# Performance work log

Measured on AMD Instinct MI355X. Metric: run time of the kernel, lower is better.

## Reference

```python
import jax, jax.numpy as jnp
import numpy as np

NINP = 850
NHID = 850
T = 128
B = 256
INITRANGE = 0.04
# DARTS published recurrent cell genotype
GENO_RECURRENT = [("sigmoid", 0), ("relu", 1), ("relu", 1), ("identity", 1),
                  ("tanh", 2), ("sigmoid", 5), ("tanh", 3), ("relu", 5)]
GENO_CONCAT = [1, 2, 3, 4, 5, 6, 7, 8]

ACT = {
    "tanh": jnp.tanh,
    "relu": jax.nn.relu,
    "sigmoid": jax.nn.sigmoid,
    "identity": lambda x: x,
}


def setup_inputs() -> dict:
    key = jax.random.key(0)
    ks = jax.random.split(key, 8)
    u = lambda k, s: jax.random.uniform(k, s, jnp.float32, -INITRANGE, INITRANGE)
    return {
        "inputs": jax.random.normal(ks[0], (T, B, NINP), jnp.float32),
        "hidden": jnp.zeros((1, B, NHID), jnp.float32),
        "W0_U": u(ks[1], (2 * NHID, 2 * NHID)),
        "W0_sigma": u(ks[2], (2 * NHID,)),
        "W0_V": u(ks[3], (2 * NHID, 2 * NHID)),
        "Ws_U": u(ks[4], (8, NHID, NHID)),
        "Ws_sigma": u(ks[5], (8, NHID)),
        "Ws_V": u(ks[6], (8, 2 * NHID, 2 * NHID)),
    }


def _lowrank_square(x, U, sig, V):
    # row == col: W = U @ diag(sig) @ V
    return ((x @ U) * sig) @ V


def _lowrank_wide(x, U, sig, V):
    # row < col (row=NHID, col=2*NHID): rectangular diag embeds rank=row into col dims
    t = (x @ U) * sig                               # [B, NHID]
    t = jnp.pad(t, ((0, 0), (0, V.shape[0] - t.shape[-1])))  # [B, 2*NHID]
    return t @ V                                    # [B, 2*NHID]


def _cell(x, h_prev, W0_U, W0_sigma, W0_V, Ws_U, Ws_sigma, Ws_V):
    xh = jnp.concatenate([x, h_prev], axis=-1)      # [B, 2*NHID]
    ch0 = _lowrank_square(xh, W0_U, W0_sigma, W0_V)  # [B, 2*NHID]
    c0 = jax.nn.sigmoid(ch0[:, :NHID])
    h0 = jnp.tanh(ch0[:, NHID:])
    s0 = h_prev + c0 * (h0 - h_prev)
    states = [s0]
    for i, (name, pred) in enumerate(GENO_RECURRENT):
        sp = states[pred]
        ch = _lowrank_wide(sp, Ws_U[i], Ws_sigma[i], Ws_V[i])
        c = jax.nn.sigmoid(ch[:, :NHID])
        hh = ACT[name](ch[:, NHID:])
        states.append(sp + c * (hh - sp))
    return jnp.mean(jnp.stack([states[i] for i in GENO_CONCAT], axis=-1), axis=-1)


def reference(inputs, hidden, W0_U, W0_sigma, W0_V, Ws_U, Ws_sigma, Ws_V):
    def step(h, x):
        h_new = _cell(x, h, W0_U, W0_sigma, W0_V, Ws_U, Ws_sigma, Ws_V)
        return h_new, h_new

    _, hiddens = jax.lax.scan(step, hidden[0], inputs)   # [T, B, NHID]
    return hiddens, hiddens[-1][None]
```

## Files before the change

kernel.cpp:

```cpp
#include <hip/hip_runtime.h>

typedef unsigned short u16;
typedef unsigned int u32;
typedef __attribute__((ext_vector_type(8))) short bf16x8;
typedef __attribute__((ext_vector_type(4))) float f32x4;

#define NHID 850
#define BATCH 256
#define TSTEPS 128
#define KPAD 896
#define KPAD0 1792

#define ACT_SIG 0
#define ACT_TANH 1
#define ACT_RELU 2
#define ACT_ID 3

__device__ __forceinline__ u16 f2bf(float f) {
  u32 u = __float_as_uint(f);
  u32 r = (u + 0x7fffu + ((u >> 16) & 1u)) >> 16;
  return (u16)r;
}
__device__ __forceinline__ float sigm(float x) { return 1.f / (1.f + __expf(-x)); }
__device__ __forceinline__ float act_apply(float x, int a) {
  if (a == ACT_SIG) return sigm(x);
  if (a == ACT_TANH) return 2.f * sigm(2.f * x) - 1.f;
  if (a == ACT_RELU) return fmaxf(x, 0.f);
  return x;
}

#define GLOAD_LDS16(gsrc, ldst)                                                     \
  __builtin_amdgcn_global_load_lds((const __attribute__((address_space(1))) void*)(gsrc), \
                                   (__attribute__((address_space(3))) void*)(ldst), 16, 0, 0)

__global__ void zero_kernel(uint4* p, u32 n) {
  u32 i = blockIdx.x * blockDim.x + threadIdx.x;
  const u32 stride = gridDim.x * blockDim.x;
  const uint4 z = {0u, 0u, 0u, 0u};
  for (; i < n; i += stride) p[i] = z;
}

__global__ void convert_kernel(const float* __restrict__ x, const float* __restrict__ h0,
                               u16* __restrict__ xb, u16* __restrict__ hb) {
  const u32 NX = (u32)TSTEPS * BATCH * NHID;
  u32 i = blockIdx.x * blockDim.x + threadIdx.x;
  if (i < NX) {
    const u32 tb = i / NHID, j = i - tb * NHID;
    xb[(size_t)tb * KPAD + j] = f2bf(x[i]);
  } else if (i < NX + (u32)BATCH * NHID) {
    const u32 k = i - NX;
    const u32 b = k / NHID, j = k - b * NHID;
    hb[(size_t)b * KPAD + j] = f2bf(h0[k]);
  }
}

__global__ __launch_bounds__(256) void prew0_kernel(const float* __restrict__ U,
                                                    const float* __restrict__ sig,
                                                    const float* __restrict__ V,
                                                    u16* __restrict__ outC,
                                                    u16* __restrict__ outH) {
  const int M = 1700, N = 1700, K = 1700;
  __shared__ float sA[64][17];
  __shared__ float sB[16][65];
  const int tid = threadIdx.x;
  const int tx = tid & 15, ty = tid >> 4;
  const int m0 = blockIdx.x * 64, n0 = blockIdx.y * 64;
  float acc[4][4] = {};
  for (int kb = 0; kb < K; kb += 16) {
#pragma unroll
    for (int i = 0; i < 4; ++i) {
      const int e = tid + i * 256;
      const int r = e >> 4, c = e & 15;
      const int mm = m0 + r, kk = kb + c;
      sA[r][c] = (mm < M && kk < K) ? U[(size_t)mm * K + kk] * sig[kk] : 0.f;
    }
#pragma unroll
    for (int i = 0; i < 4; ++i) {
      const int e = tid + i * 256;
      const int r = e >> 6, c = e & 63;
      const int kk = kb + r, nn = n0 + c;
      sB[r][c] = (kk < K && nn < N) ? V[(size_t)kk * N + nn] : 0.f;
    }
    __syncthreads();
#pragma unroll
    for (int k = 0; k < 16; ++k) {
      float a[4], b[4];
#pragma unroll
      for (int i = 0; i < 4; ++i) a[i] = sA[tx * 4 + i][k];
#pragma unroll
      for (int j = 0; j < 4; ++j) b[j] = sB[k][ty * 4 + j];
#pragma unroll
      for (int i = 0; i < 4; ++i)
#pragma unroll
        for (int j = 0; j < 4; ++j) acc[i][j] += a[i] * b[j];
    }
    __syncthreads();
  }
#pragma unroll
  for (int i = 0; i < 4; ++i) {
    const int m = m0 + tx * 4 + i;
    if (m >= M) continue;
    const int rp = (m < 850) ? m : m + 46;
#pragma unroll
    for (int j = 0; j < 4; ++j) {
      const int n = n0 + ty * 4 + j;
      if (n >= N) continue;
      if (n < 850) outC[(size_t)n * KPAD0 + rp] = f2bf(acc[i][j]);
      else outH[(size_t)(n - 850) * KPAD0 + rp] = f2bf(acc[i][j]);
    }
  }
}

__global__ __launch_bounds__(256) void prewn_kernel(const float* __restrict__ Uall,
                                                    const float* __restrict__ sigall,
                                                    const float* __restrict__ Vall,
                                                    u16* __restrict__ outBase) {
  const int M = 850, N = 1700, K = 850;
  const int ndi = blockIdx.z;
  const float* U = Uall + (size_t)ndi * 850 * 850;
  const float* sig = sigall + (size_t)ndi * 850;
  const float* V = Vall + (size_t)ndi * 1700 * 1700;
  u16* outC = outBase + (size_t)ndi * 2 * KPAD * KPAD;
  u16* outH = outC + (size_t)KPAD * KPAD;
  __shared__ float sA[64][17];
  __shared__ float sB[16][65];
  const int tid = threadIdx.x;
  const int tx = tid & 15, ty = tid >> 4;
  const int m0 = blockIdx.x * 64, n0 = blockIdx.y * 64;
  float acc[4][4] = {};
  for (int kb = 0; kb < K; kb += 16) {
#pragma unroll
    for (int i = 0; i < 4; ++i) {
      const int e = tid + i * 256;
      const int r = e >> 4, c = e & 15;
      const int mm = m0 + r, kk = kb + c;
      sA[r][c] = (mm < M && kk < K) ? U[(size_t)mm * K + kk] * sig[kk] : 0.f;
    }
#pragma unroll
    for (int i = 0; i < 4; ++i) {
      const int e = tid + i * 256;
      const int r = e >> 6, c = e & 63;
      const int kk = kb + r, nn = n0 + c;
      sB[r][c] = (kk < K && nn < N) ? V[(size_t)kk * 1700 + nn] : 0.f;
    }
    __syncthreads();
#pragma unroll
    for (int k = 0; k < 16; ++k) {
      float a[4], b[4];
#pragma unroll
      for (int i = 0; i < 4; ++i) a[i] = sA[tx * 4 + i][k];
#pragma unroll
      for (int j = 0; j < 4; ++j) b[j] = sB[k][ty * 4 + j];
#pragma unroll
      for (int i = 0; i < 4; ++i)
#pragma unroll
        for (int j = 0; j < 4; ++j) acc[i][j] += a[i] * b[j];
    }
    __syncthreads();
  }
#pragma unroll
  for (int i = 0; i < 4; ++i) {
    const int m = m0 + tx * 4 + i;
    if (m >= M) continue;
#pragma unroll
    for (int j = 0; j < 4; ++j) {
      const int n = n0 + ty * 4 + j;
      if (n >= N) continue;
      if (n < 850) outC[(size_t)n * KPAD + m] = f2bf(acc[i][j]);
      else outH[(size_t)(n - 850) * KPAD + m] = f2bf(acc[i][j]);
    }
  }
}

struct NodeDesc {
  const u16* A;
  const u16* A2;
  const u16* Bc;
  const u16* Bh;
  const float* sp;
  float* outF;
  u16* outB;
  int act;
};
struct StageArgs {
  NodeDesc d[3];
  int Kt, ktA, bStride;
};

__global__ __launch_bounds__(256) void stage_kernel(StageArgs sa) {
  const NodeDesc nd = sa.d[blockIdx.z];
  __shared__ __align__(16) u16 lA[2][4096];
  __shared__ __align__(16) u16 lBc[2][4096];
  __shared__ __align__(16) u16 lBh[2][4096];
  const int tid = threadIdx.x;
  const int lane = tid & 63;
  const int w = tid >> 6;
  const int wm = (w & 1) * 32;
  const int wn = (w >> 1) * 32;
  const int m0 = blockIdx.x * 64;
  const int n0 = blockIdx.y * 64;

  f32x4 acc[2][2][2] = {};

  auto stage = [&](int buf, int kt) {
    const u16* Asrc;
    int ktl;
    if (kt < sa.ktA) { Asrc = nd.A; ktl = kt; }
    else { Asrc = nd.A2; ktl = kt - sa.ktA; }
#pragma unroll
    for (int r2 = 0; r2 < 2; ++r2) {
      const int e = tid + 256 * r2;
      const int row = e >> 3;
      const int q = (e & 7) ^ (row & 7);
      const u16* gA = Asrc + (size_t)(m0 + row) * KPAD + ktl * 64 + q * 8;
      GLOAD_LDS16(gA, &lA[buf][e * 8]);
      const u16* gBc = nd.Bc + (size_t)(n0 + row) * sa.bStride + kt * 64 + q * 8;
      GLOAD_LDS16(gBc, &lBc[buf][e * 8]);
      const u16* gBh = nd.Bh + (size_t)(n0 + row) * sa.bStride + kt * 64 + q * 8;
      GLOAD_LDS16(gBh, &lBh[buf][e * 8]);
    }
  };

  stage(0, 0);
  int cur = 0;
  for (int kt = 0; kt < sa.Kt; ++kt) {
    __syncthreads();
    if (kt + 1 < sa.Kt) stage(cur ^ 1, kt + 1);
#pragma unroll
    for (int ks = 0; ks < 2; ++ks) {
      const int kg = lane >> 4;
      bf16x8 af[2], bc[2], bh[2];
#pragma unroll
      for (int mf = 0; mf < 2; ++mf) {
        const int row = wm + mf * 16 + (lane & 15);
        const int p = (ks * 4 + kg) ^ (row & 7);
        af[mf] = *(const bf16x8*)&lA[cur][row * 64 + p * 8];
      }
#pragma unroll
      for (int nf = 0; nf < 2; ++nf) {
        const int nr = wn + nf * 16 + (lane & 15);
        const int p = (ks * 4 + kg) ^ (nr & 7);
        bc[nf] = *(const bf16x8*)&lBc[cur][nr * 64 + p * 8];
        bh[nf] = *(const bf16x8*)&lBh[cur][nr * 64 + p * 8];
      }
#pragma unroll
      for (int mf = 0; mf < 2; ++mf)
#pragma unroll
        for (int nf = 0; nf < 2; ++nf) {
          acc[0][mf][nf] = __builtin_amdgcn_mfma_f32_16x16x32_bf16(af[mf], bc[nf], acc[0][mf][nf], 0, 0, 0);
          acc[1][mf][nf] = __builtin_amdgcn_mfma_f32_16x16x32_bf16(af[mf], bh[nf], acc[1][mf][nf], 0, 0, 0);
        }
    }
    cur ^= 1;
  }

  const int colb = n0 + wn + (lane & 15);
  const int rowb = m0 + wm + ((lane >> 4) << 2);
#pragma unroll
  for (int nf = 0; nf < 2; ++nf) {
    const int j = colb + nf * 16;
    if (j >= NHID) continue;
#pragma unroll
    for (int mf = 0; mf < 2; ++mf) {
      const int mb = rowb + mf * 16;
      const f32x4 ac = acc[0][mf][nf];
      const f32x4 ah = acc[1][mf][nf];
#pragma unroll
      for (int r = 0; r < 4; ++r) {
        const int m = mb + r;
        const float c = sigm(ac[r]);
        const float hv = act_apply(ah[r], nd.act);
        const float spv = nd.sp[m * NHID + j];
        const float s = spv + c * (hv - spv);
        nd.outF[m * NHID + j] = s;
        nd.outB[(size_t)m * KPAD + j] = f2bf(s);
      }
    }
  }
}

struct FinalArgs {
  const u16* A;
  const u16* B[4];
  const float* s1; const float* s2; const float* s3;
  const float* s4; const float* s5; const float* s7;
  float* outH;
  u16* hb;
};

__global__ __launch_bounds__(256) void final_kernel(FinalArgs fa) {
  __shared__ __align__(16) u16 lA[2][4096];
  __shared__ __align__(16) u16 lB[2][4][4096];
  const int tid = threadIdx.x;
  const int lane = tid & 63;
  const int w = tid >> 6;
  const int wm = (w & 1) * 32;
  const int wn = (w >> 1) * 32;
  const int m0 = blockIdx.x * 64;
  const int n0 = blockIdx.y * 64;

  f32x4 acc[4][2][2] = {};

  auto stage = [&](int buf, int kt) {
#pragma unroll
    for (int r2 = 0; r2 < 2; ++r2) {
      const int e = tid + 256 * r2;
      const int row = e >> 3;
      const int q = (e & 7) ^ (row & 7);
      GLOAD_LDS16(fa.A + (size_t)(m0 + row) * KPAD + kt * 64 + q * 8, &lA[buf][e * 8]);
#pragma unroll
      for (int b = 0; b < 4; ++b)
        GLOAD_LDS16(fa.B[b] + (size_t)(n0 + row) * KPAD + kt * 64 + q * 8, &lB[buf][b][e * 8]);
    }
  };

  stage(0, 0);
  int cur = 0;
  for (int kt = 0; kt < 14; ++kt) {
    __syncthreads();
    if (kt + 1 < 14) stage(cur ^ 1, kt + 1);
#pragma unroll
    for (int ks = 0; ks < 2; ++ks) {
      const int kg = lane >> 4;
      bf16x8 af[2], bb[4][2];
#pragma unroll
      for (int mf = 0; mf < 2; ++mf) {
        const int row = wm + mf * 16 + (lane & 15);
        const int p = (ks * 4 + kg) ^ (row & 7);
        af[mf] = *(const bf16x8*)&lA[cur][row * 64 + p * 8];
      }
#pragma unroll
      for (int b = 0; b < 4; ++b)
#pragma unroll
        for (int nf = 0; nf < 2; ++nf) {
          const int nr = wn + nf * 16 + (lane & 15);
          const int p = (ks * 4 + kg) ^ (nr & 7);
          bb[b][nf] = *(const bf16x8*)&lB[cur][b][nr * 64 + p * 8];
        }
#pragma unroll
      for (int b = 0; b < 4; ++b)
#pragma unroll
        for (int mf = 0; mf < 2; ++mf)
#pragma unroll
          for (int nf = 0; nf < 2; ++nf)
            acc[b][mf][nf] = __builtin_amdgcn_mfma_f32_16x16x32_bf16(af[mf], bb[b][nf], acc[b][mf][nf], 0, 0, 0);
    }
    cur ^= 1;
  }

  const int colb = n0 + wn + (lane & 15);
  const int rowb = m0 + wm + ((lane >> 4) << 2);
#pragma unroll
  for (int nf = 0; nf < 2; ++nf) {
    const int j = colb + nf * 16;
    if (j >= NHID) continue;
#pragma unroll
    for (int mf = 0; mf < 2; ++mf) {
      const int mb = rowb + mf * 16;
#pragma unroll
      for (int r = 0; r < 4; ++r) {
        const int m = mb + r;
        const int idx = m * NHID + j;
        const float s5v = fa.s5[idx];
        const float c6 = sigm(acc[0][mf][nf][r]);
        const float h6 = sigm(acc[1][mf][nf][r]);
        const float s6 = s5v + c6 * (h6 - s5v);
        const float c8 = sigm(acc[2][mf][nf][r]);
        const float h8 = fmaxf(acc[3][mf][nf][r], 0.f);
        const float s8 = s5v + c8 * (h8 - s5v);
        const float sum = fa.s1[idx] + fa.s2[idx] + fa.s3[idx] + fa.s4[idx]
                        + s5v + fa.s7[idx] + s6 + s8;
        const float h = sum * 0.125f;
        fa.outH[idx] = h;
        fa.hb[(size_t)m * KPAD + j] = f2bf(h);
      }
    }
  }
}

extern "C" void kernel_launch(void* const* d_in, const int* in_sizes, int n_in,
                              void* d_out, int out_size, void* d_ws, size_t ws_size,
                              hipStream_t stream) {
  const float* x = (const float*)d_in[0];
  const float* h0 = (const float*)d_in[1];
  const float* W0U = (const float*)d_in[2];
  const float* W0s = (const float*)d_in[3];
  const float* W0V = (const float*)d_in[4];
  const float* WsU = (const float*)d_in[5];
  const float* Wss = (const float*)d_in[6];
  const float* WsV = (const float*)d_in[7];
  float* out = (float*)d_out;
  char* ws = (char*)d_ws;

  const size_t SZ_W0HALF = (size_t)KPAD * KPAD0 * 2;
  const size_t OFF_W0C = 0, OFF_W0H = SZ_W0HALF;
  const size_t OFF_WN = 2 * SZ_W0HALF;
  const size_t SZ_WNHALF = (size_t)KPAD * KPAD * 2;
  const size_t OFF_XB = OFF_WN + 16 * SZ_WNHALF;
  const size_t SZ_XB = (size_t)TSTEPS * BATCH * KPAD * 2;
  const size_t OFF_HB = OFF_XB + SZ_XB;
  const size_t SZ_HB = (size_t)BATCH * KPAD * 2;
  const size_t OFF_SF = OFF_HB + SZ_HB;
  const size_t SZ_SF = (size_t)BATCH * NHID * 4;
  const size_t OFF_SB = OFF_SF + 9 * SZ_SF;
  const size_t SZ_SB = (size_t)BATCH * KPAD * 2;
  const size_t TOTAL = OFF_SB + 9 * SZ_SB;

  u16* w0c = (u16*)(ws + OFF_W0C);
  u16* w0h = (u16*)(ws + OFF_W0H);
  u16* wnBase = (u16*)(ws + OFF_WN);
  u16* xb = (u16*)(ws + OFF_XB);
  u16* hb = (u16*)(ws + OFF_HB);

  const size_t zbytes = (TOTAL <= ws_size) ? TOTAL : ws_size;
  zero_kernel<<<2048, 256, 0, stream>>>((uint4*)ws, (u32)(zbytes / 16));
  const u32 convTotal = (u32)TSTEPS * BATCH * NHID + (u32)BATCH * NHID;
  convert_kernel<<<(convTotal + 255) / 256, 256, 0, stream>>>(x, h0, xb, hb);
  prew0_kernel<<<dim3(27, 27), 256, 0, stream>>>(W0U, W0s, W0V, w0c, w0h);
  prewn_kernel<<<dim3(14, 27, 8), 256, 0, stream>>>(WsU, Wss, WsV, wnBase);

  auto wnc = [&](int i) { return wnBase + (size_t)i * 2 * KPAD * KPAD; };
  auto wnh = [&](int i) { return wnBase + (size_t)i * 2 * KPAD * KPAD + (size_t)KPAD * KPAD; };
  auto sf = [&](int k) { return (float*)(ws + OFF_SF + (size_t)k * SZ_SF); };
  auto sb = [&](int k) { return (u16*)(ws + OFF_SB + (size_t)k * SZ_SB); };

  for (int t = 0; t < TSTEPS; ++t) {
    const float* hprev = (t == 0) ? h0 : (out + (size_t)(t - 1) * BATCH * NHID);
    {
      StageArgs a = {};
      a.d[0] = NodeDesc{ xb + (size_t)t * BATCH * KPAD, hb, w0c, w0h, hprev, sf(0), sb(0), ACT_TANH };
      a.Kt = 28; a.ktA = 14; a.bStride = KPAD0;
      stage_kernel<<<dim3(4, 14, 1), 256, 0, stream>>>(a);
    }
    {
      StageArgs a = {};
      a.d[0] = NodeDesc{ sb(0), nullptr, wnc(0), wnh(0), sf(0), sf(1), sb(1), ACT_SIG };
      a.Kt = 14; a.ktA = 14; a.bStride = KPAD;
      stage_kernel<<<dim3(4, 14, 1), 256, 0, stream>>>(a);
    }
    {
      StageArgs a = {};
      a.d[0] = NodeDesc{ sb(1), nullptr, wnc(1), wnh(1), sf(1), sf(2), sb(2), ACT_RELU };
      a.d[1] = NodeDesc{ sb(1), nullptr, wnc(2), wnh(2), sf(1), sf(3), sb(3), ACT_RELU };
      a.d[2] = NodeDesc{ sb(1), nullptr, wnc(3), wnh(3), sf(1), sf(4), sb(4), ACT_ID };
      a.Kt = 14; a.ktA = 14; a.bStride = KPAD;
      stage_kernel<<<dim3(4, 14, 3), 256, 0, stream>>>(a);
    }
    {
      StageArgs a = {};
      a.d[0] = NodeDesc{ sb(2), nullptr, wnc(4), wnh(4), sf(2), sf(5), sb(5), ACT_TANH };
      a.d[1] = NodeDesc{ sb(3), nullptr, wnc(6), wnh(6), sf(3), sf(7), sb(7), ACT_TANH };
      a.Kt = 14; a.ktA = 14; a.bStride = KPAD;
      stage_kernel<<<dim3(4, 14, 2), 256, 0, stream>>>(a);
    }
    {
      FinalArgs f;
      f.A = sb(5);
      f.B[0] = wnc(5); f.B[1] = wnh(5); f.B[2] = wnc(7); f.B[3] = wnh(7);
      f.s1 = sf(1); f.s2 = sf(2); f.s3 = sf(3); f.s4 = sf(4); f.s5 = sf(5); f.s7 = sf(7);
      f.outH = out + (size_t)t * BATCH * NHID;
      f.hb = hb;
      final_kernel<<<dim3(4, 14), 256, 0, stream>>>(f);
    }
  }
  hipMemcpyAsync(out + (size_t)TSTEPS * BATCH * NHID,
                 out + (size_t)(TSTEPS - 1) * BATCH * NHID,
                 (size_t)BATCH * NHID * sizeof(float), hipMemcpyDeviceToDevice, stream);
}
```

Before: 15.83 ms.

## Fuse per-timestep stage kernels into one persistent kernel with grid barriers

Replaces the 5 kernel launches per timestep (640 total) with a single persistent kernel of 256 blocks that loops over timesteps and stages. An atomic-counter grid barrier separates the stages. The aim is to remove launch overhead and inter-kernel gaps on this latency-bound recurrence. In exchange, many blocks sit idle in stages that use only 56 tiles, and correctness relies on all 256 blocks being co-resident with the shared 80KB LDS footprint.

```diff
diff --git a/kernel.cpp b/kernel.cpp
--- a/kernel.cpp
+++ b/kernel.cpp
@@ -10,6 +10,7 @@
 #define TSTEPS 128
 #define KPAD 896
 #define KPAD0 1792
+#define GRIDP 256
 
 #define ACT_SIG 0
 #define ACT_TANH 1
@@ -172,60 +173,60 @@
   }
 }
 
-struct NodeDesc {
-  const u16* A;
-  const u16* A2;
-  const u16* Bc;
-  const u16* Bh;
-  const float* sp;
-  float* outF;
-  u16* outB;
-  int act;
+struct PArgs {
+  const u16* xb;
+  u16* hb;
+  const u16* w0c; const u16* w0h;
+  const u16* wnc[8]; const u16* wnh[8];
+  const float* h0;
+  float* out;
+  float* sf[8];
+  u16* sb[8];
+  u32* bar;
 };
-struct StageArgs {
-  NodeDesc d[3];
-  int Kt, ktA, bStride;
-};
-
-__global__ __launch_bounds__(256) void stage_kernel(StageArgs sa) {
-  const NodeDesc nd = sa.d[blockIdx.z];
-  __shared__ __align__(16) u16 lA[2][4096];
-  __shared__ __align__(16) u16 lBc[2][4096];
-  __shared__ __align__(16) u16 lBh[2][4096];
+
+__device__ __forceinline__ void grid_sync(u32* cnt, u32 target) {
+  __syncthreads();
+  if (threadIdx.x == 0) {
+    __hip_atomic_fetch_add(cnt, 1u, __ATOMIC_ACQ_REL, __HIP_MEMORY_SCOPE_AGENT);
+    while (__hip_atomic_load(cnt, __ATOMIC_ACQUIRE, __HIP_MEMORY_SCOPE_AGENT) < target)
+      __builtin_amdgcn_s_sleep(2);
+  }
+  __syncthreads();
+}
+
+__device__ void gemm_stage(const u16* __restrict__ A, const u16* __restrict__ A2,
+                           const u16* __restrict__ Bc, const u16* __restrict__ Bh,
+                           const float* __restrict__ sp, float* __restrict__ outF,
+                           u16* __restrict__ outB, int act, int Kt, int ktA, int bStride,
+                           int m0, int n0, u16* lds) {
   const int tid = threadIdx.x;
   const int lane = tid & 63;
   const int w = tid >> 6;
   const int wm = (w & 1) * 32;
   const int wn = (w >> 1) * 32;
-  const int m0 = blockIdx.x * 64;
-  const int n0 = blockIdx.y * 64;
-
   f32x4 acc[2][2][2] = {};
 
+  auto slot = [&](int buf, int s) { return lds + (size_t)(buf * 5 + s) * 4096; };
   auto stage = [&](int buf, int kt) {
-    const u16* Asrc;
-    int ktl;
-    if (kt < sa.ktA) { Asrc = nd.A; ktl = kt; }
-    else { Asrc = nd.A2; ktl = kt - sa.ktA; }
+    const u16* Asrc; int ktl;
+    if (kt < ktA) { Asrc = A; ktl = kt; } else { Asrc = A2; ktl = kt - ktA; }
 #pragma unroll
     for (int r2 = 0; r2 < 2; ++r2) {
       const int e = tid + 256 * r2;
       const int row = e >> 3;
       const int q = (e & 7) ^ (row & 7);
-      const u16* gA = Asrc + (size_t)(m0 + row) * KPAD + ktl * 64 + q * 8;
-      GLOAD_LDS16(gA, &lA[buf][e * 8]);
-      const u16* gBc = nd.Bc + (size_t)(n0 + row) * sa.bStride + kt * 64 + q * 8;
-      GLOAD_LDS16(gBc, &lBc[buf][e * 8]);
-      const u16* gBh = nd.Bh + (size_t)(n0 + row) * sa.bStride + kt * 64 + q * 8;
-      GLOAD_LDS16(gBh, &lBh[buf][e * 8]);
+      GLOAD_LDS16(Asrc + (size_t)(m0 + row) * KPAD + ktl * 64 + q * 8, slot(buf, 0) + e * 8);
+      GLOAD_LDS16(Bc + (size_t)(n0 + row) * bStride + kt * 64 + q * 8, slot(buf, 1) + e * 8);
+      GLOAD_LDS16(Bh + (size_t)(n0 + row) * bStride + kt * 64 + q * 8, slot(buf, 2) + e * 8);
     }
   };
 
   stage(0, 0);
   int cur = 0;
-  for (int kt = 0; kt < sa.Kt; ++kt) {
-    __syncthreads();
-    if (kt + 1 < sa.Kt) stage(cur ^ 1, kt + 1);
+  for (int kt = 0; kt < Kt; ++kt) {
+    __syncthreads();
+    if (kt + 1 < Kt) stage(cur ^ 1, kt + 1);
 #pragma unroll
     for (int ks = 0; ks < 2; ++ks) {
       const int kg = lane >> 4;
@@ -234,14 +235,14 @@
       for (int mf = 0; mf < 2; ++mf) {
         const int row = wm + mf * 16 + (lane & 15);
         const int p = (ks * 4 + kg) ^ (row & 7);
-        af[mf] = *(const bf16x8*)&lA[cur][row * 64 + p * 8];
+        af[mf] = *(const bf16x8*)(slot(cur, 0) + row * 64 + p * 8);
       }
 #pragma unroll
       for (int nf = 0; nf < 2; ++nf) {
         const int nr = wn + nf * 16 + (lane & 15);
         const int p = (ks * 4 + kg) ^ (nr & 7);
-        bc[nf] = *(const bf16x8*)&lBc[cur][nr * 64 + p * 8];
-        bh[nf] = *(const bf16x8*)&lBh[cur][nr * 64 + p * 8];
+        bc[nf] = *(const bf16x8*)(slot(cur, 1) + nr * 64 + p * 8);
+        bh[nf] = *(const bf16x8*)(slot(cur, 2) + nr * 64 + p * 8);
       }
 #pragma unroll
       for (int mf = 0; mf < 2; ++mf)
@@ -269,48 +270,37 @@
       for (int r = 0; r < 4; ++r) {
         const int m = mb + r;
         const float c = sigm(ac[r]);
-        const float hv = act_apply(ah[r], nd.act);
-        const float spv = nd.sp[m * NHID + j];
+        const float hv = act_apply(ah[r], act);
+        const float spv = sp[m * NHID + j];
         const float s = spv + c * (hv - spv);
-        nd.outF[m * NHID + j] = s;
-        nd.outB[(size_t)m * KPAD + j] = f2bf(s);
+        outF[m * NHID + j] = s;
+        outB[(size_t)m * KPAD + j] = f2bf(s);
       }
     }
   }
 }
 
-struct FinalArgs {
-  const u16* A;
-  const u16* B[4];
-  const float* s1; const float* s2; const float* s3;
-  const float* s4; const float* s5; const float* s7;
-  float* outH;
-  u16* hb;
-};
-
-__global__ __launch_bounds__(256) void final_kernel(FinalArgs fa) {
-  __shared__ __align__(16) u16 lA[2][4096];
-  __shared__ __align__(16) u16 lB[2][4][4096];
+__device__ void final_tile(const PArgs& pa, int t, int m0, int n0, u16* lds) {
   const int tid = threadIdx.x;
   const int lane = tid & 63;
   const int w = tid >> 6;
   const int wm = (w & 1) * 32;
   const int wn = (w >> 1) * 32;
-  const int m0 = blockIdx.x * 64;
-  const int n0 = blockIdx.y * 64;
-
+  const u16* A = pa.sb[5];
+  const u16* Bp[4] = { pa.wnc[5], pa.wnh[5], pa.wnc[7], pa.wnh[7] };
   f32x4 acc[4][2][2] = {};
 
+  auto slot = [&](int buf, int s) { return lds + (size_t)(buf * 5 + s) * 4096; };
   auto stage = [&](int buf, int kt) {
 #pragma unroll
     for (int r2 = 0; r2 < 2; ++r2) {
       const int e = tid + 256 * r2;
       const int row = e >> 3;
       const int q = (e & 7) ^ (row & 7);
-      GLOAD_LDS16(fa.A + (size_t)(m0 + row) * KPAD + kt * 64 + q * 8, &lA[buf][e * 8]);
+      GLOAD_LDS16(A + (size_t)(m0 + row) * KPAD + kt * 64 + q * 8, slot(buf, 0) + e * 8);
 #pragma unroll
       for (int b = 0; b < 4; ++b)
-        GLOAD_LDS16(fa.B[b] + (size_t)(n0 + row) * KPAD + kt * 64 + q * 8, &lB[buf][b][e * 8]);
+        GLOAD_LDS16(Bp[b] + (size_t)(n0 + row) * KPAD + kt * 64 + q * 8, slot(buf, 1 + b) + e * 8);
     }
   };
 
@@ -327,7 +317,7 @@
       for (int mf = 0; mf < 2; ++mf) {
         const int row = wm + mf * 16 + (lane & 15);
         const int p = (ks * 4 + kg) ^ (row & 7);
-        af[mf] = *(const bf16x8*)&lA[cur][row * 64 + p * 8];
+        af[mf] = *(const bf16x8*)(slot(cur, 0) + row * 64 + p * 8);
       }
 #pragma unroll
       for (int b = 0; b < 4; ++b)
@@ -335,7 +325,7 @@
         for (int nf = 0; nf < 2; ++nf) {
           const int nr = wn + nf * 16 + (lane & 15);
           const int p = (ks * 4 + kg) ^ (nr & 7);
-          bb[b][nf] = *(const bf16x8*)&lB[cur][b][nr * 64 + p * 8];
+          bb[b][nf] = *(const bf16x8*)(slot(cur, 1 + b) + nr * 64 + p * 8);
         }
 #pragma unroll
       for (int b = 0; b < 4; ++b)
@@ -348,6 +338,7 @@
     cur ^= 1;
   }
 
+  float* outH = pa.out + (size_t)t * BATCH * NHID;
   const int colb = n0 + wn + (lane & 15);
   const int rowb = m0 + wm + ((lane >> 4) << 2);
 #pragma unroll
@@ -361,20 +352,67 @@
       for (int r = 0; r < 4; ++r) {
         const int m = mb + r;
         const int idx = m * NHID + j;
-        const float s5v = fa.s5[idx];
+        const float s5v = pa.sf[5][idx];
         const float c6 = sigm(acc[0][mf][nf][r]);
         const float h6 = sigm(acc[1][mf][nf][r]);
         const float s6 = s5v + c6 * (h6 - s5v);
         const float c8 = sigm(acc[2][mf][nf][r]);
         const float h8 = fmaxf(acc[3][mf][nf][r], 0.f);
         const float s8 = s5v + c8 * (h8 - s5v);
-        const float sum = fa.s1[idx] + fa.s2[idx] + fa.s3[idx] + fa.s4[idx]
-                        + s5v + fa.s7[idx] + s6 + s8;
+        const float sum = pa.sf[1][idx] + pa.sf[2][idx] + pa.sf[3][idx] + pa.sf[4][idx]
+                        + s5v + pa.sf[7][idx] + s6 + s8;
         const float h = sum * 0.125f;
-        fa.outH[idx] = h;
-        fa.hb[(size_t)m * KPAD + j] = f2bf(h);
+        outH[idx] = h;
+        pa.hb[(size_t)m * KPAD + j] = f2bf(h);
       }
     }
+  }
+}
+
+__global__ __launch_bounds__(256) void cell_persist_kernel(PArgs pa) {
+  __shared__ __align__(16) u16 lds[2 * 5 * 4096];
+  const int bx = blockIdx.x;
+  const u32 nb = gridDim.x;
+  u32 gen = 0;
+
+  for (int t = 0; t < TSTEPS; ++t) {
+    const float* hprev = (t == 0) ? pa.h0 : (pa.out + (size_t)(t - 1) * BATCH * NHID);
+    if (bx < 56) {
+      const int m0 = (bx & 3) * 64, n0 = (bx >> 2) * 64;
+      gemm_stage(pa.xb + (size_t)t * BATCH * KPAD, pa.hb, pa.w0c, pa.w0h,
+                 hprev, pa.sf[0], pa.sb[0], ACT_TANH, 28, 14, KPAD0, m0, n0, lds);
+    }
+    grid_sync(pa.bar, ++gen * nb);
+    if (bx < 56) {
+      const int m0 = (bx & 3) * 64, n0 = (bx >> 2) * 64;
+      gemm_stage(pa.sb[0], nullptr, pa.wnc[0], pa.wnh[0],
+                 pa.sf[0], pa.sf[1], pa.sb[1], ACT_SIG, 14, 14, KPAD, m0, n0, lds);
+    }
+    grid_sync(pa.bar, ++gen * nb);
+    if (bx < 168) {
+      const int node = bx / 56, r = bx - node * 56;
+      const int m0 = (r & 3) * 64, n0 = (r >> 2) * 64;
+      const int act = (node == 2) ? ACT_ID : ACT_RELU;
+      gemm_stage(pa.sb[1], nullptr, pa.wnc[1 + node], pa.wnh[1 + node],
+                 pa.sf[1], pa.sf[2 + node], pa.sb[2 + node], act, 14, 14, KPAD, m0, n0, lds);
+    }
+    grid_sync(pa.bar, ++gen * nb);
+    if (bx < 112) {
+      const int g = bx / 56, r = bx - g * 56;
+      const int m0 = (r & 3) * 64, n0 = (r >> 2) * 64;
+      if (g == 0)
+        gemm_stage(pa.sb[2], nullptr, pa.wnc[4], pa.wnh[4],
+                   pa.sf[2], pa.sf[5], pa.sb[5], ACT_TANH, 14, 14, KPAD, m0, n0, lds);
+      else
+        gemm_stage(pa.sb[3], nullptr, pa.wnc[6], pa.wnh[6],
+                   pa.sf[3], pa.sf[7], pa.sb[7], ACT_TANH, 14, 14, KPAD, m0, n0, lds);
+    }
+    grid_sync(pa.bar, ++gen * nb);
+    if (bx < 56) {
+      const int m0 = (bx & 3) * 64, n0 = (bx >> 2) * 64;
+      final_tile(pa, t, m0, n0, lds);
+    }
+    grid_sync(pa.bar, ++gen * nb);
   }
 }
 
@@ -402,9 +440,10 @@
   const size_t SZ_HB = (size_t)BATCH * KPAD * 2;
   const size_t OFF_SF = OFF_HB + SZ_HB;
   const size_t SZ_SF = (size_t)BATCH * NHID * 4;
-  const size_t OFF_SB = OFF_SF + 9 * SZ_SF;
+  const size_t OFF_SB = OFF_SF + 8 * SZ_SF;
   const size_t SZ_SB = (size_t)BATCH * KPAD * 2;
-  const size_t TOTAL = OFF_SB + 9 * SZ_SB;
+  const size_t OFF_BAR = OFF_SB + 8 * SZ_SB;
+  const size_t TOTAL = OFF_BAR + 128;
 
   u16* w0c = (u16*)(ws + OFF_W0C);
   u16* w0h = (u16*)(ws + OFF_W0H);
@@ -413,56 +452,31 @@
   u16* hb = (u16*)(ws + OFF_HB);
 
   const size_t zbytes = (TOTAL <= ws_size) ? TOTAL : ws_size;
-  zero_kernel<<<2048, 256, 0, stream>>>((uint4*)ws, (u32)(zbytes / 16));
+  zero_kernel<<<2048, 256, 0, stream>>>((uint4*)ws, (u32)((zbytes + 15) / 16));
   const u32 convTotal = (u32)TSTEPS * BATCH * NHID + (u32)BATCH * NHID;
   convert_kernel<<<(convTotal + 255) / 256, 256, 0, stream>>>(x, h0, xb, hb);
   prew0_kernel<<<dim3(27, 27), 256, 0, stream>>>(W0U, W0s, W0V, w0c, w0h);
   prewn_kernel<<<dim3(14, 27, 8), 256, 0, stream>>>(WsU, Wss, WsV, wnBase);
 
-  auto wnc = [&](int i) { return wnBase + (size_t)i * 2 * KPAD * KPAD; };
-  auto wnh = [&](int i) { return wnBase + (size_t)i * 2 * KPAD * KPAD + (size_t)KPAD * KPAD; };
-  auto sf = [&](int k) { return (float*)(ws + OFF_SF + (size_t)k * SZ_SF); };
-  auto sb = [&](int k) { return (u16*)(ws + OFF_SB + (size_t)k * SZ_SB); };
-
-  for (int t = 0; t < TSTEPS; ++t) {
-    const float* hprev = (t == 0) ? h0 : (out + (size_t)(t - 1) * BATCH * NHID);
-    {
-      StageArgs a = {};
-      a.d[0] = NodeDesc{ xb + (size_t)t * BATCH * KPAD, hb, w0c, w0h, hprev, sf(0), sb(0), ACT_TANH };
-      a.Kt = 28; a.ktA = 14; a.bStride = KPAD0;
-      stage_kernel<<<dim3(4, 14, 1), 256, 0, stream>>>(a);
-    }
-    {
-      StageArgs a = {};
-      a.d[0] = NodeDesc{ sb(0), nullptr, wnc(0), wnh(0), sf(0), sf(1), sb(1), ACT_SIG };
-      a.Kt = 14; a.ktA = 14; a.bStride = KPAD;
-      stage_kernel<<<dim3(4, 14, 1), 256, 0, stream>>>(a);
-    }
-    {
-      StageArgs a = {};
-      a.d[0] = NodeDesc{ sb(1), nullptr, wnc(1), wnh(1), sf(1), sf(2), sb(2), ACT_RELU };
-      a.d[1] = NodeDesc{ sb(1), nullptr, wnc(2), wnh(2), sf(1), sf(3), sb(3), ACT_RELU };
-      a.d[2] = NodeDesc{ sb(1), nullptr, wnc(3), wnh(3), sf(1), sf(4), sb(4), ACT_ID };
-      a.Kt = 14; a.ktA = 14; a.bStride = KPAD;
-      stage_kernel<<<dim3(4, 14, 3), 256, 0, stream>>>(a);
-    }
-    {
-      StageArgs a = {};
-      a.d[0] = NodeDesc{ sb(2), nullptr, wnc(4), wnh(4), sf(2), sf(5), sb(5), ACT_TANH };
-      a.d[1] = NodeDesc{ sb(3), nullptr, wnc(6), wnh(6), sf(3), sf(7), sb(7), ACT_TANH };
-      a.Kt = 14; a.ktA = 14; a.bStride = KPAD;
-      stage_kernel<<<dim3(4, 14, 2), 256, 0, stream>>>(a);
-    }
-    {
-      FinalArgs f;
-      f.A = sb(5);
-      f.B[0] = wnc(5); f.B[1] = wnh(5); f.B[2] = wnc(7); f.B[3] = wnh(7);
-      f.s1 = sf(1); f.s2 = sf(2); f.s3 = sf(3); f.s4 = sf(4); f.s5 = sf(5); f.s7 = sf(7);
-      f.outH = out + (size_t)t * BATCH * NHID;
-      f.hb = hb;
-      final_kernel<<<dim3(4, 14), 256, 0, stream>>>(f);
-    }
-  }
+  PArgs pa;
+  pa.xb = xb;
+  pa.hb = hb;
+  pa.w0c = w0c;
+  pa.w0h = w0h;
+  for (int i = 0; i < 8; ++i) {
+    pa.wnc[i] = wnBase + (size_t)i * 2 * KPAD * KPAD;
+    pa.wnh[i] = wnBase + (size_t)i * 2 * KPAD * KPAD + (size_t)KPAD * KPAD;
+  }
+  pa.h0 = h0;
+  pa.out = out;
+  for (int i = 0; i < 8; ++i) {
+    pa.sf[i] = (float*)(ws + OFF_SF + (size_t)i * SZ_SF);
+    pa.sb[i] = (u16*)(ws + OFF_SB + (size_t)i * SZ_SB);
+  }
+  pa.bar = (u32*)(ws + OFF_BAR);
+
+  cell_persist_kernel<<<GRIDP, 256, 0, stream>>>(pa);
+
   hipMemcpyAsync(out + (size_t)TSTEPS * BATCH * NHID,
                  out + (size_t)(TSTEPS - 1) * BATCH * NHID,
                  (size_t)BATCH * NHID * sizeof(float), hipMemcpyDeviceToDevice, stream);
```

Result: slower. 60.30 ms (+281.0%).
